# Kernel tuning notes

Measured on AMD Instinct MI355X. Metric: run time of the kernel, lower is better.

Reference implementation:

```python
import jax, jax.numpy as jnp
import numpy as np
from jax.ops import segment_sum, segment_max

H = 64          # hidden_dim
HEADS = 4       # GAT heads (concat=False -> mean over heads)
N_VAR = 500_000
N_EMP = 3_000
N_SHIFT = 30_000
N_CON = 50_000
E_SD = 960_000
E_VE = 500_000
E_VS = 500_000
F_EMP, F_SHIFT, F_VAR, F_CON = 32, 24, 19, 5


def setup_inputs() -> dict:
    key = jax.random.key(0)
    ks = jax.random.split(key, 32)
    def g(i, shape):
        return jax.random.normal(ks[i], shape, jnp.float32) * 0.05
    return dict(
        x_emp=jax.random.normal(ks[0], (N_EMP, F_EMP), jnp.float32),
        x_shift=jax.random.normal(ks[1], (N_SHIFT, F_SHIFT), jnp.float32),
        x_var=jax.random.normal(ks[2], (N_VAR, F_VAR), jnp.float32),
        x_con=jax.random.normal(ks[3], (N_CON, F_CON), jnp.float32),
        W_emp=g(4, (F_EMP, H)), b_emp=jnp.zeros((H,), jnp.float32),
        W_shift=g(5, (F_SHIFT, H)), b_shift=jnp.zeros((H,), jnp.float32),
        W_var=g(6, (F_VAR, H)), b_var=jnp.zeros((H,), jnp.float32),
        W_con=g(7, (F_CON, H)), b_con=jnp.zeros((H,), jnp.float32),
        gat_W=g(8, (H, HEADS * H)), gat_att_src=g(9, (HEADS, H)),
        gat_att_dst=g(10, (HEADS, H)), gat_b=jnp.zeros((H,), jnp.float32),
        injW_emp=g(11, (H, H)), injb_emp=jnp.zeros((H,), jnp.float32),
        injW_shift=g(12, (H, H)), injb_shift=jnp.zeros((H,), jnp.float32),
        qW_emp=g(13, (H, H)), kW_emp=g(14, (H, H)),
        qW_shift=g(15, (H, H)), kW_shift=g(16, (H, H)),
        fuseW=g(17, (3 * H, H)), fuseb=jnp.zeros((H,), jnp.float32),
        sd_src=jax.random.randint(ks[18], (E_SD,), 0, N_SHIFT),
        sd_dst=jax.random.randint(ks[19], (E_SD,), 0, N_SHIFT),
        ve_var=jax.random.randint(ks[20], (E_VE,), 0, N_VAR),
        ve_emp=jax.random.randint(ks[21], (E_VE,), 0, N_EMP),
        vs_var=jax.random.randint(ks[22], (E_VS,), 0, N_VAR),
        vs_shift=jax.random.randint(ks[23], (E_VS,), 0, N_SHIFT),
    )


def _gat(h, W, att_src, att_dst, bias, src, dst):
    # PyG GATConv, heads=HEADS, concat=False, no self-loops, eval mode (no dropout)
    n = h.shape[0]
    x = (h @ W).reshape(n, HEADS, H)                    # [S, heads, H]
    a_s = jnp.einsum('nhd,hd->nh', x, att_src)          # [S, heads]
    a_d = jnp.einsum('nhd,hd->nh', x, att_dst)
    e = jax.nn.leaky_relu(a_s[src] + a_d[dst], 0.2)     # [E, heads]
    m = segment_max(e, dst, num_segments=n)
    ex = jnp.exp(e - m[dst])
    z = segment_sum(ex, dst, num_segments=n)
    alpha = ex / jnp.maximum(z[dst], 1e-16)             # scatter-softmax per dst node
    out = segment_sum(x[src] * alpha[:, :, None], dst, num_segments=n)
    return out.mean(axis=1) + bias                      # concat=False -> head mean


def _inject(h_var, h_ent, injW, injb, qW, kW, dst, src):
    # gather Q/K/V per edge -> dot score -> segment softmax over variables -> scatter-sum
    scale = jnp.sqrt(jnp.float32(H))
    vals = (h_ent @ injW + injb)[src]                   # [E, H]
    q = (h_var @ qW)[dst]                               # [E, H]
    k = (h_ent @ kW)[src]                               # [E, H]
    s = jnp.sum(q * k, axis=-1) / scale                 # [E]
    m = segment_max(s, dst, num_segments=N_VAR)
    e = jnp.exp(s - m[dst])
    z = jnp.maximum(segment_sum(e, dst, num_segments=N_VAR), 1e-9)
    alpha = e / z[dst]
    return segment_sum(vals * alpha[:, None], dst, num_segments=N_VAR)


def reference(x_emp, x_shift, x_var, x_con,
              W_emp, b_emp, W_shift, b_shift, W_var, b_var, W_con, b_con,
              gat_W, gat_att_src, gat_att_dst, gat_b,
              injW_emp, injb_emp, injW_shift, injb_shift,
              qW_emp, kW_emp, qW_shift, kW_shift, fuseW, fuseb,
              sd_src, sd_dst, ve_var, ve_emp, vs_var, vs_shift):
    # Stage 0: project all node types to hidden_dim
    h_emp = jax.nn.relu(x_emp @ W_emp + b_emp)
    h_shift = jax.nn.relu(x_shift @ W_shift + b_shift)
    h_var = jax.nn.relu(x_var @ W_var + b_var)
    h_con = jax.nn.relu(x_con @ W_con + b_con)  # projected but unused downstream
    # Stage 1: one HeteroConv layer = GAT on Shift same_day edges, relu + residual
    gat_out = _gat(h_shift, gat_W, gat_att_src, gat_att_dst, gat_b, sd_src, sd_dst)
    h_shift = jax.nn.relu(gat_out) + h_shift
    # Stage 2: semantic injection into variable nodes
    msg_e = _inject(h_var, h_emp, injW_emp, injb_emp, qW_emp, kW_emp, ve_var, ve_emp)
    msg_s = _inject(h_var, h_shift, injW_shift, injb_shift, qW_shift, kW_shift, vs_var, vs_shift)
    fused = jnp.concatenate([h_var, msg_e, msg_s], axis=-1)  # [N_var, 3H]
    h_var_new = jax.nn.relu(fused @ fuseW + fuseb)
    return jnp.sqrt(jnp.sum(h_var_new * h_var_new, axis=-1))  # L2 norm pseudo-scores
```

## Files before the change

### kernel.cpp

```cpp
#include <hip/hip_runtime.h>
#include <math.h>

#define NEMP   3000
#define NSHIFT 30000
#define NVAR   500000
#define ESD    960000
#define EVE    500000
#define EVS    500000
#define NT_CNT (NSHIFT + NVAR + NVAR)
#define ET_ALL (ESD + EVE + EVS)

#define NBUCK  959
#define NBLK0  256
#define CHUNK  7657
#define SSTRIDE 7664
#define SBIAS  250152960

#define S2CAP  384
#define GCAP   1536

typedef __attribute__((ext_vector_type(8))) short short8;
typedef __attribute__((ext_vector_type(4))) float f32x4;

__device__ __forceinline__ unsigned short f2bf(float x) {
  unsigned u = __float_as_uint(x);
  unsigned r = (u + 0x7FFFu + ((u >> 16) & 1u)) >> 16;
  return (unsigned short)r;
}
__device__ __forceinline__ float bf2f(unsigned short u) {
  return __uint_as_float((unsigned)u << 16);
}
__device__ __forceinline__ int swz(int r, int f) {
  return (((f >> 3) ^ (r & 7)) << 3) | (f & 7);
}
__device__ __forceinline__ int kvoff(int j, int isV) {
  return ((j >> 2) << 3) | (isV << 2) | (j & 3);
}

__device__ __forceinline__ void edge_decode(int i,
    const int* __restrict__ sd_dst, const int* __restrict__ sd_src,
    const int* __restrict__ ve_var, const int* __restrict__ ve_emp,
    const int* __restrict__ vs_var, const int* __restrict__ vs_shift,
    int& b, unsigned& packed) {
  if (i < ESD)            { int d = sd_dst[i]; b = d >> 6; packed = (unsigned)(d & 63) | ((unsigned)sd_src[i] << 11); }
  else if (i < ESD + EVE) { int j = i - ESD; int d = ve_var[j]; b = 469 + (d >> 11); packed = (unsigned)(d & 2047) | ((unsigned)ve_emp[j] << 11); }
  else                    { int j = i - ESD - EVE; int d = vs_var[j]; b = 714 + (d >> 11); packed = (unsigned)(d & 2047) | ((unsigned)vs_shift[j] << 11); }
}

__device__ __forceinline__ void qkfold_body(const float* __restrict__ qW,
    const float* __restrict__ kW, float* __restrict__ W2,
    unsigned short* __restrict__ W2frag) {
  int j = threadIdx.x & 63;
  int fq = threadIdx.x >> 6;
  for (int ff = 0; ff < 8; ++ff) {
    int f = fq * 8 + ff;
    float acc = 0.0f;
    #pragma unroll
    for (int d = 0; d < 64; ++d) acc = fmaf(qW[j * 64 + d], kW[f * 64 + d], acc);
    float val = 0.125f * acc;
    if (W2) W2[f * 64 + j] = val;
    if (W2frag) {
      int kb = f >> 5;
      int lane = (((f & 31) >> 3) << 4) | (j & 15);
      int ntile = j >> 4;
      W2frag[((((ntile << 1) + kb) * 64 + lane) << 3) | (f & 7)] = f2bf(val);
    }
  }
}

__global__ __launch_bounds__(512) void prep_bin_proj_kernel(
    const float* __restrict__ qWe, const float* __restrict__ kWe,
    const float* __restrict__ qWs, const float* __restrict__ kWs,
    const float* __restrict__ fuseW, const float* __restrict__ gat_W,
    const float* __restrict__ att_src, const float* __restrict__ att_dst,
    const float* __restrict__ W_var, const float* __restrict__ injW_s,
    float* __restrict__ W2e, unsigned short* __restrict__ W2sb,
    unsigned short* __restrict__ injWsb,
    unsigned short* __restrict__ fuseWb,
    float* __restrict__ w_as, float* __restrict__ w_ad,
    unsigned short* __restrict__ Wrb, unsigned short* __restrict__ Wvb,
    const int* __restrict__ sd_dst, const int* __restrict__ sd_src,
    const int* __restrict__ ve_var, const int* __restrict__ ve_emp,
    const int* __restrict__ vs_var, const int* __restrict__ vs_shift,
    unsigned* __restrict__ staging, int* __restrict__ table,
    const float* __restrict__ x_emp, const float* __restrict__ W_emp,
    const float* __restrict__ b_emp, float* __restrict__ h_emp,
    const float* __restrict__ x_shift, const float* __restrict__ W_shift,
    const float* __restrict__ b_shift, unsigned short* __restrict__ h_sh0b,
    float* __restrict__ a_s, float* __restrict__ a_d) {
  __shared__ int hist[NBUCK];
  __shared__ int sums[512];
  __shared__ unsigned pkc[CHUNK];
  __shared__ unsigned short bkc[CHUNK];
  int t = threadIdx.x;
  int bx = blockIdx.x;
  if (bx < 7) {
    if (bx == 0) { qkfold_body(qWe, kWe, W2e, nullptr); return; }
    if (bx == 1) { qkfold_body(qWs, kWs, nullptr, W2sb); return; }
    if (bx == 2) {
      for (int linear = t; linear < 192 * 64; linear += 512) {
        int i    = linear & 7;
        int lane = (linear >> 3) & 63;
        int g    = linear >> 9;
        int kb   = g % 6, nt = g / 6;
        int k = kb * 32 + (lane >> 4) * 8 + i;
        int n = nt * 16 + (lane & 15);
        fuseWb[linear] = f2bf(fuseW[k * 64 + n]);
      }
      return;
    }
    if (bx == 3) {
      if (t < 256) {
        int h = t >> 6, f = t & 63;
        float as = 0.0f, ad = 0.0f;
        #pragma unroll
        for (int d = 0; d < 64; ++d) {
          float wv = gat_W[f * 256 + h * 64 + d];
          as = fmaf(wv, att_src[h * 64 + d], as);
          ad = fmaf(wv, att_dst[h * 64 + d], ad);
        }
        w_as[f * 4 + h] = as;
        w_ad[f * 4 + h] = ad;
      }
      return;
    }
    if (bx == 4) {
      for (int linear = t; linear < 4 * 8 * 64 * 8; linear += 512) {
        int i    = linear & 7;
        int lane = (linear >> 3) & 63;
        int g    = linear >> 9;
        int kb   = g & 7, nt = g >> 3;
        int k = kb * 32 + ((lane >> 4) << 3) + i;
        int j = nt * 16 + (lane & 15);
        Wrb[linear] = f2bf(0.25f * gat_W[(k & 63) * 256 + (k >> 6) * 64 + j]);
      }
      return;
    }
    if (bx == 5) {
      for (int linear = t; linear < 4 * 64 * 8; linear += 512) {
        int i    = linear & 7;
        int lane = (linear >> 3) & 63;
        int nt   = linear >> 9;
        int k = ((lane >> 4) << 3) + i;
        int j = nt * 16 + (lane & 15);
        Wvb[linear] = (k < 19) ? f2bf(W_var[k * 64 + j]) : (unsigned short)0;
      }
      return;
    }
    for (int linear = t; linear < 4 * 2 * 64 * 8; linear += 512) {
      int i    = linear & 7;
      int lane = (linear >> 3) & 63;
      int g    = linear >> 9;
      int kb   = g & 1, nt = g >> 1;
      int k = kb * 32 + ((lane >> 4) << 3) + i;
      int j = nt * 16 + (lane & 15);
      injWsb[linear] = f2bf(injW_s[k * 64 + j]);
    }
    return;
  }
  if (bx >= 263) {
    int j = t & 63;
    if (bx < 638) {
      int n = __builtin_amdgcn_readfirstlane((int)((bx - 263) * 8 + (t >> 6)));
      if (n >= NEMP) return;
      const float* xr = x_emp + (size_t)n * 32;
      float acc = b_emp[j];
      #pragma unroll
      for (int f = 0; f < 32; ++f) acc = fmaf(xr[f], W_emp[f * 64 + j], acc);
      h_emp[(size_t)n * 64 + j] = fmaxf(acc, 0.0f);
      return;
    }
    int n = __builtin_amdgcn_readfirstlane((int)((bx - 638) * 8 + (t >> 6)));
    if (n >= NSHIFT) return;
    const float* xr = x_shift + (size_t)n * 24;
    float acc = b_shift[j];
    #pragma unroll
    for (int f = 0; f < 24; ++f) acc = fmaf(xr[f], W_shift[f * 64 + j], acc);
    float h = fmaxf(acc, 0.0f);
    h_sh0b[(size_t)n * 64 + j] = f2bf(h);
    const float4 was4 = *(const float4*)(w_as + j * 4);
    const float4 wad4 = *(const float4*)(w_ad + j * 4);
    float s0 = h * was4.x, s1 = h * was4.y, s2 = h * was4.z, s3 = h * was4.w;
    float d0 = h * wad4.x, d1 = h * wad4.y, d2 = h * wad4.z, d3 = h * wad4.w;
    #pragma unroll
    for (int o = 32; o > 0; o >>= 1) {
      s0 += __shfl_xor(s0, o); s1 += __shfl_xor(s1, o);
      s2 += __shfl_xor(s2, o); s3 += __shfl_xor(s3, o);
      d0 += __shfl_xor(d0, o); d1 += __shfl_xor(d1, o);
      d2 += __shfl_xor(d2, o); d3 += __shfl_xor(d3, o);
    }
    if (j == 0) {
      *(float4*)(a_s + n * 4) = make_float4(s0, s1, s2, s3);
      *(float4*)(a_d + n * 4) = make_float4(d0, d1, d2, d3);
    }
    return;
  }
  int blk = bx - 7;
  int e0 = blk * CHUNK;
  int e1 = min(e0 + CHUNK, ET_ALL);
  int sbase = blk * SSTRIDE;
  for (int i = t; i < NBUCK; i += 512) hist[i] = 0;
  __syncthreads();
  for (int i = e0 + t; i < e1; i += 512) {
    int b; unsigned pk;
    edge_decode(i, sd_dst, sd_src, ve_var, ve_emp, vs_var, vs_shift, b, pk);
    pkc[i - e0] = pk;
    bkc[i - e0] = (unsigned short)b;
    atomicAdd(&hist[b], 1);
  }
  __syncthreads();
  int base = t * 2, v[2], s = 0;
  #pragma unroll
  for (int k = 0; k < 2; ++k) { int i = base + k; v[k] = (i < NBUCK) ? hist[i] : 0; s += v[k]; }
  sums[t] = s; __syncthreads();
  for (int o = 1; o < 512; o <<= 1) {
    int add = (t >= o) ? sums[t - o] : 0;
    __syncthreads(); sums[t] += add; __syncthreads();
  }
  int run = sums[t] - s;
  #pragma unroll
  for (int k = 0; k < 2; ++k) {
    int i = base + k;
    if (i < NBUCK) { hist[i] = run; table[i * NBLK0 + blk] = sbase + run; run += v[k]; }
  }
  if (t == 0) table[NBUCK * NBLK0 + blk] = sbase + (e1 - e0);
  __syncthreads();
  for (int i = e0 + t; i < e1; i += 512) {
    int b = bkc[i - e0];
    int pos = sbase + atomicAdd(&hist[b], 1);
    staging[pos] = pkc[i - e0];
  }
}

__global__ __launch_bounds__(256) void csr_linemp_kernel(
    const unsigned* __restrict__ staging, const int* __restrict__ table,
    int* __restrict__ row, int* __restrict__ elist,
    const float* __restrict__ h_emp, const float* __restrict__ injW_e,
    const float* __restrict__ injb_e, const float* __restrict__ W2e,
    unsigned short* __restrict__ KVe) {
  __shared__ int hist[2048];
  __shared__ int sums[256];
  int bx = blockIdx.x, t = threadIdx.x;
  if (bx >= NBUCK) {
    int b = bx - NBUCK;
    const float *W, *bias; int isV, nb;
    if (b < 750) { W = injW_e; bias = injb_e;  isV = 1; nb = b; }
    else         { W = W2e;    bias = nullptr; isV = 0; nb = b - 750; }
    int n = __builtin_amdgcn_readfirstlane((int)(nb * 4 + (t >> 6)));
    int j = t & 63;
    if (n >= NEMP) return;
    const float* hr = h_emp + (size_t)n * 64;
    float acc = bias ? bias[j] : 0.0f;
    #pragma unroll
    for (int f = 0; f < 64; ++f) acc = fmaf(hr[f], W[f * 64 + j], acc);
    KVe[(n << 7) | kvoff(j, isV)] = f2bf(acc);
    return;
  }
  int b = bx;
  int s0 = table[b * NBLK0 + t];
  int s1 = table[(b + 1) * NBLK0 + t];
  sums[t] = s0; __syncthreads();
  for (int o = 128; o > 0; o >>= 1) { if (t < o) sums[t] += sums[t + o]; __syncthreads(); }
  int bs = sums[0] - SBIAS;
  int totAll = 0;
  if (b == NBUCK - 1) {
    __syncthreads();
    sums[t] = s1; __syncthreads();
    for (int o = 128; o > 0; o >>= 1) { if (t < o) sums[t] += sums[t + o]; __syncthreads(); }
    totAll = sums[0] - SBIAS;
  }
  __syncthreads();
  for (int i = t; i < 2048; i += 256) hist[i] = 0;
  __syncthreads();
  for (int p = s0; p < s1; ++p) atomicAdd(&hist[staging[p] & 2047u], 1);
  __syncthreads();
  int keyBase, kcount;
  if (b < 469)      { keyBase = b * 64;                     kcount = min(64,   30000  - b * 64); }
  else if (b < 714) { int lb = b - 469; keyBase = 30000  + lb * 2048; kcount = min(2048, 500000 - lb * 2048); }
  else              { int lb = b - 714; keyBase = 530000 + lb * 2048; kcount = min(2048, 500000 - lb * 2048); }
  int base = t * 8, v[8], s = 0;
  #pragma unroll
  for (int k = 0; k < 8; ++k) { int i = base + k; v[k] = (i < kcount) ? hist[i] : 0; s += v[k]; }
  sums[t] = s; __syncthreads();
  for (int o = 1; o < 256; o <<= 1) {
    int add = (t >= o) ? sums[t - o] : 0;
    __syncthreads(); sums[t] += add; __syncthreads();
  }
  int run = sums[t] - s;
  #pragma unroll
  for (int k = 0; k < 8; ++k) {
    int i = base + k;
    if (i < kcount) { hist[i] = run; row[keyBase + i] = bs + run; run += v[k]; }
  }
  if (b == NBUCK - 1 && t == 0) row[NT_CNT] = totAll;
  __syncthreads();
  for (int p = s0; p < s1; ++p) {
    unsigned pr = staging[p];
    int pos = bs + atomicAdd(&hist[pr & 2047u], 1);
    elist[pos] = (int)(pr >> 11);
  }
}

__global__ __launch_bounds__(512) void gat_kernel(
    const unsigned short* __restrict__ h_sh0b,
    const float* __restrict__ a_s, const float* __restrict__ a_d,
    const int* __restrict__ row, const int* __restrict__ elist,
    const unsigned short* __restrict__ Wrb, const float* __restrict__ gat_b,
    const unsigned short* __restrict__ W2sb, const unsigned short* __restrict__ injWsb,
    const float* __restrict__ injb_s,
    unsigned short* __restrict__ KVs) {
  __shared__ unsigned short aggTn[32][256];
  __shared__ __attribute__((aligned(16))) unsigned short hb[32][64];
  __shared__ int elG[GCAP];
  __shared__ int rowLocG[33];
  int tid = threadIdx.x;
  int bx = blockIdx.x;
  int lane = tid & 63;
  int w = __builtin_amdgcn_readfirstlane((int)(tid >> 6));
  int blockStart = bx * 32;
  if (tid < 33) rowLocG[tid] = row[min(blockStart + tid, NSHIFT)];
  __syncthreads();
  int baseG = rowLocG[0];
  int lenG = min(rowLocG[32] - baseG, GCAP);
  for (int i = tid; i < lenG; i += 512) elG[i] = elist[baseG + i];
  __syncthreads();

  for (int k = 0; k < 4; ++k) {
    int c = w * 4 + k;
    int n = blockStart + c;
    float4 ad4 = make_float4(0.f, 0.f, 0.f, 0.f);
    if (n < NSHIFT) ad4 = *(const float4*)(a_d + (n << 2));
    int lb = rowLocG[c] - baseG, le = rowLocG[c + 1] - baseG;
    float g0 = 0, g1 = 0, g2 = 0, g3 = 0, z0 = 0, z1 = 0, z2 = 0, z3 = 0;
    int p = lb;
    for (; p + 2 <= le; p += 2) {
      int s0 = elG[p], s1 = elG[p + 1];
      const float4 asA = *(const float4*)(a_s + (s0 << 2));
      const float4 asB = *(const float4*)(a_s + (s1 << 2));
      float hvA = bf2f(h_sh0b[(s0 << 6) | lane]);
      float hvB = bf2f(h_sh0b[(s1 << 6) | lane]);
      float a0 = asA.x + ad4.x, a1 = asA.y + ad4.y, a2 = asA.z + ad4.z, a3 = asA.w + ad4.w;
      float b0 = asB.x + ad4.x, b1 = asB.y + ad4.y, b2 = asB.z + ad4.z, b3 = asB.w + ad4.w;
      a0 = a0 > 0.f ? a0 : 0.2f * a0;  a1 = a1 > 0.f ? a1 : 0.2f * a1;
      a2 = a2 > 0.f ? a2 : 0.2f * a2;  a3 = a3 > 0.f ? a3 : 0.2f * a3;
      b0 = b0 > 0.f ? b0 : 0.2f * b0;  b1 = b1 > 0.f ? b1 : 0.2f * b1;
      b2 = b2 > 0.f ? b2 : 0.2f * b2;  b3 = b3 > 0.f ? b3 : 0.2f * b3;
      float xA0 = __expf(a0), xA1 = __expf(a1), xA2 = __expf(a2), xA3 = __expf(a3);
      float xB0 = __expf(b0), xB1 = __expf(b1), xB2 = __expf(b2), xB3 = __expf(b3);
      z0 += xA0 + xB0; z1 += xA1 + xB1; z2 += xA2 + xB2; z3 += xA3 + xB3;
      g0 = fmaf(xA0, hvA, fmaf(xB0, hvB, g0));
      g1 = fmaf(xA1, hvA, fmaf(xB1, hvB, g1));
      g2 = fmaf(xA2, hvA, fmaf(xB2, hvB, g2));
      g3 = fmaf(xA3, hvA, fmaf(xB3, hvB, g3));
    }
    if (p < le) {
      int s0 = elG[p];
      const float4 asA = *(const float4*)(a_s + (s0 << 2));
      float hvA = bf2f(h_sh0b[(s0 << 6) | lane]);
      float a0 = asA.x + ad4.x, a1 = asA.y + ad4.y, a2 = asA.z + ad4.z, a3 = asA.w + ad4.w;
      a0 = a0 > 0.f ? a0 : 0.2f * a0;  a1 = a1 > 0.f ? a1 : 0.2f * a1;
      a2 = a2 > 0.f ? a2 : 0.2f * a2;  a3 = a3 > 0.f ? a3 : 0.2f * a3;
      float xA0 = __expf(a0), xA1 = __expf(a1), xA2 = __expf(a2), xA3 = __expf(a3);
      z0 += xA0; z1 += xA1; z2 += xA2; z3 += xA3;
      g0 = fmaf(xA0, hvA, g0); g1 = fmaf(xA1, hvA, g1);
      g2 = fmaf(xA2, hvA, g2); g3 = fmaf(xA3, hvA, g3);
    }
    aggTn[c][swz(c, lane)]       = f2bf(g0 / fmaxf(z0, 1e-16f));
    aggTn[c][swz(c, 64 + lane)]  = f2bf(g1 / fmaxf(z1, 1e-16f));
    aggTn[c][swz(c, 128 + lane)] = f2bf(g2 / fmaxf(z2, 1e-16f));
    aggTn[c][swz(c, 192 + lane)] = f2bf(g3 / fmaxf(z3, 1e-16f));
  }
  __syncthreads();

  {
    int mtile = w >> 2, ntile = w & 3;
    int row16 = lane & 15, blk4 = lane >> 4;
    int mrow = mtile * 16 + row16;
    f32x4 acc = {0.f, 0.f, 0.f, 0.f};
    #pragma unroll
    for (int kb = 0; kb < 8; ++kb) {
      short8 a = *(const short8*)&aggTn[mrow][swz(mrow, kb * 32 + blk4 * 8)];
      short8 bfr = *(const short8*)(Wrb + (((ntile * 8 + kb) * 64 + lane) << 3));
      acc = __builtin_amdgcn_mfma_f32_16x16x32_bf16(a, bfr, acc, 0, 0, 0);
    }
    int j = ntile * 16 + row16;
    float gb = gat_b[j];
    #pragma unroll
    for (int r = 0; r < 4; ++r) {
      int nl = mtile * 16 + blk4 * 4 + r;
      int node = blockStart + nl;
      float o = 0.0f;
      if (node < NSHIFT)
        o = fmaxf(acc[r] + gb, 0.0f) + bf2f(h_sh0b[((size_t)node << 6) | j]);
      hb[nl][swz(nl, j)] = f2bf(o);
    }
  }
  __syncthreads();

  {
    int mat = w & 1;
    int mtile = (w >> 1) & 1;
    int npair = w >> 2;
    const unsigned short* Wfrag = mat ? injWsb : W2sb;
    int row16 = lane & 15, blk4 = lane >> 4;
    int mrow = mtile * 16 + row16;
    #pragma unroll
    for (int tt = 0; tt < 2; ++tt) {
      int ntile = npair * 2 + tt;
      f32x4 acc = {0.f, 0.f, 0.f, 0.f};
      #pragma unroll
      for (int kb = 0; kb < 2; ++kb) {
        short8 a = *(const short8*)&hb[mrow][swz(mrow, kb * 32 + blk4 * 8)];
        short8 bfr = *(const short8*)(Wfrag + (((ntile * 2 + kb) * 64 + lane) << 3));
        acc = __builtin_amdgcn_mfma_f32_16x16x32_bf16(a, bfr, acc, 0, 0, 0);
      }
      int j = ntile * 16 + row16;
      float bias = mat ? injb_s[j] : 0.0f;
      #pragma unroll
      for (int r = 0; r < 4; ++r) {
        int node = blockStart + mtile * 16 + blk4 * 4 + r;
        if (node < NSHIFT)
          KVs[(node << 7) | kvoff(j, mat)] = f2bf(acc[r] + bias);
      }
    }
  }
}

__global__ __launch_bounds__(512) void stage2_kernel(
    const float* __restrict__ x_var, const unsigned short* __restrict__ Wvb,
    const float* __restrict__ b_var,
    const unsigned short* __restrict__ KVe, const int* __restrict__ ve_row,
    const unsigned short* __restrict__ KVs, const int* __restrict__ vs_row,
    const int* __restrict__ elist,
    const unsigned short* __restrict__ fuseWb, const float* __restrict__ fuseb,
    float* __restrict__ out, int N) {
  __shared__ __attribute__((aligned(16))) unsigned short fTn[64][192];
  __shared__ __attribute__((aligned(16))) unsigned short xb[64][40];
  __shared__ int elE[S2CAP], elS[S2CAP];
  __shared__ int rowLocE[65], rowLocS[65];
  __shared__ float ssq2[64][2];
  int tid = threadIdx.x;
  int lane = tid & 63;
  int w = __builtin_amdgcn_readfirstlane((int)(tid >> 6));
  int sl = lane & 15;
  int blockStart = blockIdx.x * 64;

  if (tid < 65) {
    int nn = min(blockStart + tid, N);
    rowLocE[tid] = ve_row[nn];
    rowLocS[tid] = vs_row[nn];
  }
  {
    int r = tid >> 3, k = tid & 7;
    int n = blockStart + r;
    bool act = (n < N);
    const float* xr = x_var + (size_t)n * 19;
    float v0 = act ? xr[k] : 0.0f;
    float v1 = act ? xr[8 + k] : 0.0f;
    float v2 = (act && k < 3) ? xr[16 + k] : 0.0f;
    xb[r][k] = f2bf(v0);
    xb[r][8 + k] = f2bf(v1);
    xb[r][16 + k] = (k < 3) ? f2bf(v2) : (unsigned short)0;
    xb[r][24 + k] = 0;
  }
  __syncthreads();

  int baseE = rowLocE[0], baseS = rowLocS[0];
  int lenE = min(rowLocE[64] - baseE, S2CAP);
  int lenS = min(rowLocS[64] - baseS, S2CAP);
  for (int i = tid; i < lenE; i += 512) elE[i] = elist[baseE + i];
  for (int i = tid; i < lenS; i += 512) elS[i] = elist[baseS + i];

  {
    int mtile = w >> 1;
    int mrow = mtile * 16 + sl;
    short8 a = *(const short8*)&xb[mrow][(lane >> 4) * 8];
    #pragma unroll
    for (int t = 0; t < 2; ++t) {
      int ntile = (w & 1) * 2 + t;
      short8 bfr = *(const short8*)(Wvb + ((ntile * 64 + lane) << 3));
      f32x4 acc = {0.f, 0.f, 0.f, 0.f};
      acc = __builtin_amdgcn_mfma_f32_16x16x32_bf16(a, bfr, acc, 0, 0, 0);
      int dim = ntile * 16 + sl;
      float bv = b_var[dim];
      #pragma unroll
      for (int r = 0; r < 4; ++r) {
        int node = mtile * 16 + (lane >> 4) * 4 + r;
        fTn[node][swz(node, dim)] = f2bf(fmaxf(acc[r] + bv, 0.0f));
      }
    }
  }
  __syncthreads();

  {
    int g = lane >> 4;
    int sl4 = sl << 2;
    int sl8 = sl << 3;
    #pragma unroll
    for (int k = 0; k < 4; ++k) {
      int task = k * 4 + g;
      bool typS = task >= 8;
      int c = w * 8 + (task & 7);
      const unsigned short* KV = typS ? KVs : KVe;
      const int* rowLoc = typS ? rowLocS : rowLocE;
      const int* elL = typS ? elS : elE;
      int bb = typS ? baseS : baseE;
      int outBase = typS ? 128 : 64;
      int lb = rowLoc[c] - bb, le = rowLoc[c + 1] - bb;
      int deg = le - lb;
      ushort4 msgb = make_ushort4(0, 0, 0, 0);
      if (deg == 1) {
        msgb = *(const ushort4*)(KV + ((elL[lb] << 7) | sl8 | 4));
      } else if (deg > 1) {
        const ushort4 hu = *(const ushort4*)&fTn[c][swz(c, sl4)];
        float4 hv = make_float4(bf2f(hu.x), bf2f(hu.y), bf2f(hu.z), bf2f(hu.w));
        float z = 0.0f;
        float4 acc = make_float4(0.f, 0.f, 0.f, 0.f);
        int p = lb;
        for (; p + 2 <= le; p += 2) {
          short8 kv0 = *(const short8*)(KV + ((elL[p] << 7) | sl8));
          short8 kv1 = *(const short8*)(KV + ((elL[p + 1] << 7) | sl8));
          float p0 = hv.x * bf2f((unsigned short)kv0[0]) + hv.y * bf2f((unsigned short)kv0[1])
                   + hv.z * bf2f((unsigned short)kv0[2]) + hv.w * bf2f((unsigned short)kv0[3]);
          float p1 = hv.x * bf2f((unsigned short)kv1[0]) + hv.y * bf2f((unsigned short)kv1[1])
                   + hv.z * bf2f((unsigned short)kv1[2]) + hv.w * bf2f((unsigned short)kv1[3]);
          p0 += __shfl_xor(p0, 1); p1 += __shfl_xor(p1, 1);
          p0 += __shfl_xor(p0, 2); p1 += __shfl_xor(p1, 2);
          p0 += __shfl_xor(p0, 4); p1 += __shfl_xor(p1, 4);
          p0 += __shfl_xor(p0, 8); p1 += __shfl_xor(p1, 8);
          float e0 = __expf(p0), e1 = __expf(p1);
          z += e0 + e1;
          acc.x = fmaf(e0, bf2f((unsigned short)kv0[4]), fmaf(e1, bf2f((unsigned short)kv1[4]), acc.x));
          acc.y = fmaf(e0, bf2f((unsigned short)kv0[5]), fmaf(e1, bf2f((unsigned short)kv1[5]), acc.y));
          acc.z = fmaf(e0, bf2f((unsigned short)kv0[6]), fmaf(e1, bf2f((unsigned short)kv1[6]), acc.z));
          acc.w = fmaf(e0, bf2f((unsigned short)kv0[7]), fmaf(e1, bf2f((unsigned short)kv1[7]), acc.w));
        }
        if (p < le) {
          short8 kv0 = *(const short8*)(KV + ((elL[p] << 7) | sl8));
          float p0 = hv.x * bf2f((unsigned short)kv0[0]) + hv.y * bf2f((unsigned short)kv0[1])
                   + hv.z * bf2f((unsigned short)kv0[2]) + hv.w * bf2f((unsigned short)kv0[3]);
          p0 += __shfl_xor(p0, 1); p0 += __shfl_xor(p0, 2);
          p0 += __shfl_xor(p0, 4); p0 += __shfl_xor(p0, 8);
          float e0 = __expf(p0);
          z += e0;
          acc.x = fmaf(e0, bf2f((unsigned short)kv0[4]), acc.x);
          acc.y = fmaf(e0, bf2f((unsigned short)kv0[5]), acc.y);
          acc.z = fmaf(e0, bf2f((unsigned short)kv0[6]), acc.z);
          acc.w = fmaf(e0, bf2f((unsigned short)kv0[7]), acc.w);
        }
        float inv = 1.0f / fmaxf(z, 1e-9f);
        msgb = make_ushort4(f2bf(acc.x * inv), f2bf(acc.y * inv),
                            f2bf(acc.z * inv), f2bf(acc.w * inv));
      }
      *(ushort4*)&fTn[c][swz(c, outBase + sl4)] = msgb;
    }
  }
  __syncthreads();

  {
    int mtile = w >> 1;
    int row16 = lane & 15, blk = lane >> 4;
    int mrow = mtile * 16 + row16;
    float nodeSS[4] = {0.f, 0.f, 0.f, 0.f};
    #pragma unroll
    for (int t = 0; t < 2; ++t) {
      int ntile = (w & 1) * 2 + t;
      f32x4 acc = {0.f, 0.f, 0.f, 0.f};
      #pragma unroll
      for (int kb = 0; kb < 6; ++kb) {
        short8 a = *(const short8*)&fTn[mrow][swz(mrow, kb * 32 + blk * 8)];
        short8 bfr = *(const short8*)(fuseWb + (((ntile * 6 + kb) * 64 + lane) << 3));
        acc = __builtin_amdgcn_mfma_f32_16x16x32_bf16(a, bfr, acc, 0, 0, 0);
      }
      float fb = fuseb[ntile * 16 + row16];
      #pragma unroll
      for (int r = 0; r < 4; ++r) {
        float v = fmaxf(acc[r] + fb, 0.0f);
        float vv = v * v;
        vv += __shfl_xor(vv, 1); vv += __shfl_xor(vv, 2);
        vv += __shfl_xor(vv, 4); vv += __shfl_xor(vv, 8);
        nodeSS[r] += vv;
      }
    }
    if (row16 == 0) {
      #pragma unroll
      for (int r = 0; r < 4; ++r)
        ssq2[mtile * 16 + blk * 4 + r][w & 1] = nodeSS[r];
    }
  }
  __syncthreads();
  if (tid < 64) {
    int n = blockStart + tid;
    if (n < N) out[n] = sqrtf(ssq2[tid][0] + ssq2[tid][1]);
  }
}

extern "C" void kernel_launch(void* const* d_in, const int* in_sizes, int n_in,
                              void* d_out, int out_size, void* d_ws, size_t ws_size,
                              hipStream_t stream) {
  const float* x_emp   = (const float*)d_in[0];
  const float* x_shift = (const float*)d_in[1];
  const float* x_var   = (const float*)d_in[2];
  const float* W_emp   = (const float*)d_in[4];
  const float* b_emp   = (const float*)d_in[5];
  const float* W_shift = (const float*)d_in[6];
  const float* b_shift = (const float*)d_in[7];
  const float* W_var   = (const float*)d_in[8];
  const float* b_var   = (const float*)d_in[9];
  const float* gat_W   = (const float*)d_in[12];
  const float* att_s   = (const float*)d_in[13];
  const float* att_d   = (const float*)d_in[14];
  const float* gat_b   = (const float*)d_in[15];
  const float* injW_e  = (const float*)d_in[16];
  const float* injb_e  = (const float*)d_in[17];
  const float* injW_s  = (const float*)d_in[18];
  const float* injb_s  = (const float*)d_in[19];
  const float* qW_e    = (const float*)d_in[20];
  const float* kW_e    = (const float*)d_in[21];
  const float* qW_s    = (const float*)d_in[22];
  const float* kW_s    = (const float*)d_in[23];
  const float* fuseW   = (const float*)d_in[24];
  const float* fuseb   = (const float*)d_in[25];
  const int* sd_src  = (const int*)d_in[26];
  const int* sd_dst  = (const int*)d_in[27];
  const int* ve_var  = (const int*)d_in[28];
  const int* ve_emp  = (const int*)d_in[29];
  const int* vs_var  = (const int*)d_in[30];
  const int* vs_shift= (const int*)d_in[31];
  float* out = (float*)d_out;

  char* base = (char*)d_ws;
  size_t off = 0;
  auto A = [&](size_t nbytes) -> void* {
    void* r = base + off;
    off = (off + nbytes + 255) & ~(size_t)255;
    return r;
  };
  float* h_emp = (float*)A((size_t)NEMP * 64 * 4);
  unsigned short* h_sh0b = (unsigned short*)A((size_t)NSHIFT * 64 * 2);
  float* a_s   = (float*)A((size_t)NSHIFT * 4 * 4);
  float* a_d   = (float*)A((size_t)NSHIFT * 4 * 4);
  unsigned short* KVe = (unsigned short*)A((size_t)NEMP * 128 * 2);
  unsigned short* KVs = (unsigned short*)A((size_t)NSHIFT * 128 * 2);
  float* W2e   = (float*)A((size_t)64 * 64 * 4);
  unsigned short* W2sb   = (unsigned short*)A((size_t)4 * 2 * 64 * 8 * 2);
  unsigned short* injWsb = (unsigned short*)A((size_t)4 * 2 * 64 * 8 * 2);
  float* w_as  = (float*)A((size_t)64 * 4 * 4);
  float* w_ad  = (float*)A((size_t)64 * 4 * 4);
  unsigned short* fuseWb = (unsigned short*)A((size_t)192 * 64 * 2);
  unsigned short* Wrb    = (unsigned short*)A((size_t)256 * 64 * 2);
  unsigned short* Wvb    = (unsigned short*)A((size_t)4 * 64 * 8 * 2);
  int* row_all = (int*)A((size_t)(NT_CNT + 1) * 4);
  int* el_all  = (int*)A((size_t)ET_ALL * 4);
  unsigned* staging = (unsigned*)A((size_t)NBLK0 * SSTRIDE * 4);
  int* table   = (int*)A((size_t)(NBUCK + 1) * NBLK0 * 4);

  prep_bin_proj_kernel<<<7 + NBLK0 + 375 + 3750, 512, 0, stream>>>(
      qW_e, kW_e, qW_s, kW_s, fuseW, gat_W, att_s, att_d, W_var, injW_s,
      W2e, W2sb, injWsb, fuseWb, w_as, w_ad, Wrb, Wvb,
      sd_dst, sd_src, ve_var, ve_emp, vs_var, vs_shift,
      staging, table,
      x_emp, W_emp, b_emp, h_emp,
      x_shift, W_shift, b_shift, h_sh0b,
      a_s, a_d);

  csr_linemp_kernel<<<NBUCK + 1500, 256, 0, stream>>>(
      staging, table, row_all, el_all,
      h_emp, injW_e, injb_e, W2e, KVe);

  gat_kernel<<<938, 512, 0, stream>>>(
      h_sh0b, a_s, a_d, row_all, el_all, Wrb, gat_b,
      W2sb, injWsb, injb_s, KVs);

  stage2_kernel<<<(NVAR + 63) / 64, 512, 0, stream>>>(x_var, Wvb, b_var,
      KVe, row_all + NSHIFT,
      KVs, row_all + NSHIFT + NVAR,
      el_all, fuseWb, fuseb, out, NVAR);
}
```

Before: 269.6 us.

## Defer var-edge CSR buckets into GAT kernel to overlap with GAT work

Factors the per-bucket CSR build into a templated device function. The CSR kernel now builds only the shift same-day buckets, and the variable-edge buckets (employee and shift injection) run as extra 512-thread blocks appended to the GAT kernel launch. This takes CSR work off the critical path before GAT so it overlaps with GAT blocks. GAT's row lookup for the last entry is hardcoded to ESD, since row[NSHIFT] may not be written yet when GAT blocks read it.

```diff
diff --git a/kernel.cpp b/kernel.cpp
--- a/kernel.cpp
+++ b/kernel.cpp
@@ -11,6 +11,7 @@
 #define ET_ALL (ESD + EVE + EVS)
 
 #define NBUCK  959
+#define NSDB   469
 #define NBLK0  256
 #define CHUNK  7657
 #define SSTRIDE 7664
@@ -45,6 +46,61 @@
   if (i < ESD)            { int d = sd_dst[i]; b = d >> 6; packed = (unsigned)(d & 63) | ((unsigned)sd_src[i] << 11); }
   else if (i < ESD + EVE) { int j = i - ESD; int d = ve_var[j]; b = 469 + (d >> 11); packed = (unsigned)(d & 2047) | ((unsigned)ve_emp[j] << 11); }
   else                    { int j = i - ESD - EVE; int d = vs_var[j]; b = 714 + (d >> 11); packed = (unsigned)(d & 2047) | ((unsigned)vs_shift[j] << 11); }
+}
+
+template<int NT>
+__device__ __forceinline__ void csr_bucket_body(int b,
+    const unsigned* __restrict__ staging, const int* __restrict__ table,
+    int* __restrict__ row, int* __restrict__ elist) {
+  __shared__ int hist[2048];
+  __shared__ int sums[NT];
+  int t = threadIdx.x;
+  int s0 = 0, s1 = 0;
+  if (t < NBLK0) {
+    s0 = table[b * NBLK0 + t];
+    s1 = table[(b + 1) * NBLK0 + t];
+  }
+  sums[t] = s0; __syncthreads();
+  for (int o = NT / 2; o > 0; o >>= 1) { if (t < o) sums[t] += sums[t + o]; __syncthreads(); }
+  int bs = sums[0] - SBIAS;
+  int totAll = 0;
+  if (b == NBUCK - 1) {
+    __syncthreads();
+    sums[t] = s1; __syncthreads();
+    for (int o = NT / 2; o > 0; o >>= 1) { if (t < o) sums[t] += sums[t + o]; __syncthreads(); }
+    totAll = sums[0] - SBIAS;
+  }
+  __syncthreads();
+  for (int i = t; i < 2048; i += NT) hist[i] = 0;
+  __syncthreads();
+  for (int p = s0; p < s1; ++p) atomicAdd(&hist[staging[p] & 2047u], 1);
+  __syncthreads();
+  int keyBase, kcount;
+  if (b < 469)      { keyBase = b * 64;                     kcount = min(64,   30000  - b * 64); }
+  else if (b < 714) { int lb = b - 469; keyBase = 30000  + lb * 2048; kcount = min(2048, 500000 - lb * 2048); }
+  else              { int lb = b - 714; keyBase = 530000 + lb * 2048; kcount = min(2048, 500000 - lb * 2048); }
+  constexpr int ITEMS = 2048 / NT;
+  int base = t * ITEMS, v[ITEMS], s = 0;
+  #pragma unroll
+  for (int k = 0; k < ITEMS; ++k) { int i = base + k; v[k] = (i < kcount) ? hist[i] : 0; s += v[k]; }
+  sums[t] = s; __syncthreads();
+  for (int o = 1; o < NT; o <<= 1) {
+    int add = (t >= o) ? sums[t - o] : 0;
+    __syncthreads(); sums[t] += add; __syncthreads();
+  }
+  int run = sums[t] - s;
+  #pragma unroll
+  for (int k = 0; k < ITEMS; ++k) {
+    int i = base + k;
+    if (i < kcount) { hist[i] = run; row[keyBase + i] = bs + run; run += v[k]; }
+  }
+  if (b == NBUCK - 1 && t == 0) row[NT_CNT] = totAll;
+  __syncthreads();
+  for (int p = s0; p < s1; ++p) {
+    unsigned pr = staging[p];
+    int pos = bs + atomicAdd(&hist[pr & 2047u], 1);
+    elist[pos] = (int)(pr >> 11);
+  }
 }
 
 __device__ __forceinline__ void qkfold_body(const float* __restrict__ qW,
@@ -238,11 +294,9 @@
     const float* __restrict__ h_emp, const float* __restrict__ injW_e,
     const float* __restrict__ injb_e, const float* __restrict__ W2e,
     unsigned short* __restrict__ KVe) {
-  __shared__ int hist[2048];
-  __shared__ int sums[256];
   int bx = blockIdx.x, t = threadIdx.x;
-  if (bx >= NBUCK) {
-    int b = bx - NBUCK;
+  if (bx >= NSDB) {
+    int b = bx - NSDB;
     const float *W, *bias; int isV, nb;
     if (b < 750) { W = injW_e; bias = injb_e;  isV = 1; nb = b; }
     else         { W = W2e;    bias = nullptr; isV = 0; nb = b - 750; }
@@ -256,69 +310,35 @@
     KVe[(n << 7) | kvoff(j, isV)] = f2bf(acc);
     return;
   }
-  int b = bx;
-  int s0 = table[b * NBLK0 + t];
-  int s1 = table[(b + 1) * NBLK0 + t];
-  sums[t] = s0; __syncthreads();
-  for (int o = 128; o > 0; o >>= 1) { if (t < o) sums[t] += sums[t + o]; __syncthreads(); }
-  int bs = sums[0] - SBIAS;
-  int totAll = 0;
-  if (b == NBUCK - 1) {
-    __syncthreads();
-    sums[t] = s1; __syncthreads();
-    for (int o = 128; o > 0; o >>= 1) { if (t < o) sums[t] += sums[t + o]; __syncthreads(); }
-    totAll = sums[0] - SBIAS;
-  }
-  __syncthreads();
-  for (int i = t; i < 2048; i += 256) hist[i] = 0;
-  __syncthreads();
-  for (int p = s0; p < s1; ++p) atomicAdd(&hist[staging[p] & 2047u], 1);
-  __syncthreads();
-  int keyBase, kcount;
-  if (b < 469)      { keyBase = b * 64;                     kcount = min(64,   30000  - b * 64); }
-  else if (b < 714) { int lb = b - 469; keyBase = 30000  + lb * 2048; kcount = min(2048, 500000 - lb * 2048); }
-  else              { int lb = b - 714; keyBase = 530000 + lb * 2048; kcount = min(2048, 500000 - lb * 2048); }
-  int base = t * 8, v[8], s = 0;
-  #pragma unroll
-  for (int k = 0; k < 8; ++k) { int i = base + k; v[k] = (i < kcount) ? hist[i] : 0; s += v[k]; }
-  sums[t] = s; __syncthreads();
-  for (int o = 1; o < 256; o <<= 1) {
-    int add = (t >= o) ? sums[t - o] : 0;
-    __syncthreads(); sums[t] += add; __syncthreads();
-  }
-  int run = sums[t] - s;
-  #pragma unroll
-  for (int k = 0; k < 8; ++k) {
-    int i = base + k;
-    if (i < kcount) { hist[i] = run; row[keyBase + i] = bs + run; run += v[k]; }
-  }
-  if (b == NBUCK - 1 && t == 0) row[NT_CNT] = totAll;
-  __syncthreads();
-  for (int p = s0; p < s1; ++p) {
-    unsigned pr = staging[p];
-    int pos = bs + atomicAdd(&hist[pr & 2047u], 1);
-    elist[pos] = (int)(pr >> 11);
-  }
-}
-
-__global__ __launch_bounds__(512) void gat_kernel(
+  csr_bucket_body<256>(bx, staging, table, row, elist);
+}
+
+__global__ __launch_bounds__(512) void gat_csr_kernel(
     const unsigned short* __restrict__ h_sh0b,
     const float* __restrict__ a_s, const float* __restrict__ a_d,
-    const int* __restrict__ row, const int* __restrict__ elist,
+    int* __restrict__ row, int* __restrict__ elist,
     const unsigned short* __restrict__ Wrb, const float* __restrict__ gat_b,
     const unsigned short* __restrict__ W2sb, const unsigned short* __restrict__ injWsb,
     const float* __restrict__ injb_s,
-    unsigned short* __restrict__ KVs) {
+    unsigned short* __restrict__ KVs,
+    const unsigned* __restrict__ staging, const int* __restrict__ table) {
   __shared__ unsigned short aggTn[32][256];
   __shared__ __attribute__((aligned(16))) unsigned short hb[32][64];
   __shared__ int elG[GCAP];
   __shared__ int rowLocG[33];
   int tid = threadIdx.x;
   int bx = blockIdx.x;
+  if (bx >= 938) {
+    csr_bucket_body<512>(NSDB + (bx - 938), staging, table, row, elist);
+    return;
+  }
   int lane = tid & 63;
   int w = __builtin_amdgcn_readfirstlane((int)(tid >> 6));
   int blockStart = bx * 32;
-  if (tid < 33) rowLocG[tid] = row[min(blockStart + tid, NSHIFT)];
+  if (tid < 33) {
+    int idx = blockStart + tid;
+    rowLocG[tid] = (idx >= NSHIFT) ? ESD : row[idx];
+  }
   __syncthreads();
   int baseG = rowLocG[0];
   int lenG = min(rowLocG[32] - baseG, GCAP);
@@ -664,13 +684,13 @@
       x_shift, W_shift, b_shift, h_sh0b,
       a_s, a_d);
 
-  csr_linemp_kernel<<<NBUCK + 1500, 256, 0, stream>>>(
+  csr_linemp_kernel<<<NSDB + 1500, 256, 0, stream>>>(
       staging, table, row_all, el_all,
       h_emp, injW_e, injb_e, W2e, KVe);
 
-  gat_kernel<<<938, 512, 0, stream>>>(
+  gat_csr_kernel<<<938 + (NBUCK - NSDB), 512, 0, stream>>>(
       h_sh0b, a_s, a_d, row_all, el_all, Wrb, gat_b,
-      W2sb, injWsb, injb_s, KVs);
+      W2sb, injWsb, injb_s, KVs, staging, table);
 
   stage2_kernel<<<(NVAR + 63) / 64, 512, 0, stream>>>(x_var, Wvb, b_var,
       KVe, row_all + NSHIFT,
```

After: 254.1 us. -5.8%, faster.
